# Optimization experiments

Hardware: AMD Instinct MI355X
Metric: run time of the kernel (lower is better)

## Reference

```python
import jax, jax.numpy as jnp
import numpy as np

B, T = 8, 5
C2, C1, C0 = 128, 256, 512  # in_channels = [C2, C1, C0]


def _ln(x, g, b):
    # LayerNorm over last (channel) axis
    m = jnp.mean(x, axis=-1, keepdims=True)
    v = jnp.var(x, axis=-1, keepdims=True)
    return (x - m) * jax.lax.rsqrt(v + 1e-5) * g + b


def _fuse_branch(x, gc, bc, gr, br, Wcur, Wref, bf, convw, bns, bnb):
    # x: [B, C, T, H, W]
    xt = jnp.transpose(x, (0, 2, 3, 4, 1))            # [B, T, H, W, C] (channel-last, like the permutes)
    cur = xt[:, -1]                                    # [B, H, W, C] last frame
    refs = xt[:, :-1]                                  # [B, T-1, H, W, C]
    # ShiftVSS stand-in: cross-frame fuse with residual (vectorized over T-1 frames)
    cur_proj = jnp.einsum('bhwc,cd->bhwd', _ln(cur, gc, bc), Wcur)        # [B,H,W,C]
    ref_proj = jnp.einsum('bthwc,cd->bthwd', _ln(refs, gr, br), Wref)     # [B,T-1,H,W,C]
    h = cur[:, None] + jax.nn.silu(cur_proj[:, None] + ref_proj + bf)     # [B,T-1,H,W,C]
    # BaseConv 1x1: pointwise conv + folded-BN + SiLU
    y = jax.nn.silu(jnp.einsum('bthwc,cd->bthwd', h, convw) * bns + bnb)  # [B,T-1,H,W,C]
    # fused temporal max + avg pooling (AdaptiveMax/AvgPool3d to T=1)
    pooled = jnp.max(y, axis=1) + jnp.mean(y, axis=1)                     # [B,H,W,C]
    return jnp.transpose(pooled, (0, 3, 1, 2))                            # [B,C,H,W]


def setup_inputs() -> dict:
    key = jax.random.key(0)
    ks = jax.random.split(key, 32)

    def n(k, shape, s=1.0):
        return jax.random.normal(k, shape, dtype=jnp.float32) * s

    d = {}
    d['x2'] = n(ks[0], (B, C2, T, 64, 64))
    d['x1'] = n(ks[1], (B, C1, T, 32, 32))
    d['x0'] = n(ks[2], (B, C0, T, 16, 16))  # unused by forward, kept for signature fidelity
    for i, (p, C) in enumerate([('2', C2), ('1', C1)]):
        o = 3 + i * 4
        d[f'g{p}c'] = jnp.ones((C,), jnp.float32)
        d[f'b{p}c'] = jnp.zeros((C,), jnp.float32)
        d[f'g{p}r'] = jnp.ones((C,), jnp.float32)
        d[f'b{p}r'] = jnp.zeros((C,), jnp.float32)
        d[f'W{p}cur'] = n(ks[o], (C, C), 0.02)
        d[f'W{p}ref'] = n(ks[o + 1], (C, C), 0.02)
        d[f'bias{p}'] = jnp.zeros((C,), jnp.float32)
        d[f'convw{p}'] = n(ks[o + 2], (C, C), 0.02)
        d[f'bns{p}'] = jnp.ones((C,), jnp.float32)
        d[f'bnb{p}'] = jnp.zeros((C,), jnp.float32)
    return d


def reference(x2, x1, x0,
              g2c, b2c, g2r, b2r, W2cur, W2ref, bias2, convw2, bns2, bnb2,
              g1c, b1c, g1r, b1r, W1cur, W1ref, bias1, convw1, bns1, bnb1):
    x2_out = _fuse_branch(x2, g2c, b2c, g2r, b2r, W2cur, W2ref, bias2, convw2, bns2, bnb2)
    x1_out = _fuse_branch(x1, g1c, b1c, g1r, b1r, W1cur, W1ref, bias1, convw1, bns1, bnb1)
    return (x2_out, x1_out)
```

## Files before the change

kernel.cpp:

```cpp
#include <hip/hip_runtime.h>
#include <stdint.h>

#define DI __device__ __forceinline__

typedef __attribute__((ext_vector_type(8))) short short8;
typedef __attribute__((ext_vector_type(4))) float f32x4;

DI float bf2f(unsigned short u){ union{unsigned int i; float f;} v; v.i = ((unsigned int)u)<<16; return v.f; }
DI unsigned short f2bf(float f){ union{float f; unsigned int i;} v; v.f=f; return (unsigned short)((v.i + 0x7fffu + ((v.i>>16)&1u))>>16); }
DI float siluf(float x){ return x/(1.f + __expf(-x)); }
DI f32x4 vzero(){ f32x4 z; z[0]=0.f;z[1]=0.f;z[2]=0.f;z[3]=0.f; return z; }
DI f32x4 vsplat(float x){ f32x4 z; z[0]=x;z[1]=x;z[2]=x;z[3]=x; return z; }

struct PrepArgs {
  const float* W[6];
  const float* g[6];
  unsigned short* Wt[6];
  int C[6];
};

__global__ __launch_bounds__(256) void prep_transpose(PrepArgs a){
  int m = blockIdx.z;
  int C = a.C[m];
  int nt = C >> 5;
  if ((int)blockIdx.x >= nt || (int)blockIdx.y >= nt) return;
  __shared__ float tile[32][33];
  int col = threadIdx.x & 31;
  int rr  = threadIdx.x >> 5;
  const float* W = a.W[m];
  const float* g = a.g[m];
  #pragma unroll
  for (int p=0;p<4;++p){
    int r = rr + p*8;
    int cK = blockIdx.x*32 + r;
    int dN = blockIdx.y*32 + col;
    float v = W[(size_t)cK*C + dN];
    if (g) v *= g[cK];
    tile[r][col] = v;
  }
  __syncthreads();
  unsigned short* Wt = a.Wt[m];
  #pragma unroll
  for (int p=0;p<4;++p){
    int r = rr + p*8;
    int dN = blockIdx.y*32 + r;
    int cK = blockIdx.x*32 + col;
    Wt[(size_t)dN*C + cK] = f2bf(tile[col][r]);
  }
}

struct ColArgs {
  const float* W[4]; const float* g[4]; const float* b[4]; const float* extra[4];
  float* ocs[4]; float* obs[4]; int C[4];
};

__global__ __launch_bounds__(256) void prep_colsum(ColArgs a){
  int j = blockIdx.y;
  int C = a.C[j];
  int d0 = blockIdx.x * 64;
  if (d0 >= C) return;
  int dl = threadIdx.x & 63;
  int g  = threadIdx.x >> 6;
  int d  = d0 + dl;
  const float* W = a.W[j]; const float* gv = a.g[j]; const float* bv = a.b[j];
  float cs = 0.f, bs = 0.f;
  for (int c = g; c < C; c += 4){
    float gc = gv[c], bc = bv[c];
    float w = W[(size_t)c*C + d];
    cs += gc*w;
    bs += bc*w;
  }
  __shared__ float rcs[4][64], rbs[4][64];
  rcs[g][dl] = cs; rbs[g][dl] = bs;
  __syncthreads();
  if (threadIdx.x < 64){
    float c0 = rcs[0][dl]+rcs[1][dl]+rcs[2][dl]+rcs[3][dl];
    float b0 = rbs[0][dl]+rbs[1][dl]+rbs[2][dl]+rbs[3][dl];
    if (a.extra[j]) b0 += a.extra[j][d];
    a.ocs[j][d] = c0;
    a.obs[j][d] = b0;
  }
}

template<int C, int PX>
__global__ __launch_bounds__(256) void fusedv5(
    const float* __restrict__ x,
    const unsigned short* __restrict__ WtCur,
    const unsigned short* __restrict__ WtRef,
    const unsigned short* __restrict__ WtConv,
    const float* __restrict__ colC, const float* __restrict__ biasC,
    const float* __restrict__ colR, const float* __restrict__ biasR,
    const float* __restrict__ bns, const float* __restrict__ bnb,
    float* __restrict__ out, int HW){
  constexpr int T = 5;
  constexpr int DSPAN = C/4;
  constexpr int NF = DSPAN/16;
  constexpr int MF = PX/16;
  constexpr int KS = C/32;
  constexpr int G = 256/PX;
  constexpr int PER = (C/8)/G;
  constexpr int PQn = PX/4;
  constexpr int ABYTES = PX*2*C;
  constexpr int POOLB = PX*(C+1)*4;
  constexpr int LDS_TOT = (ABYTES + 2048 + PX*8 > POOLB) ? (ABYTES + 2048 + PX*8) : POOLB;

  __shared__ __align__(16) char L[LDS_TOT];
  float* red = (float*)(L + ABYTES);
  float* smean = (float*)(L + ABYTES + 2048);
  float* srstd = smean + PX;

  int px0 = blockIdx.x*PX;
  int b = px0 / HW, hw0 = px0 % HW;
  int tid = threadIdx.x, lane = tid&63, wc = tid>>6;
  int cl = lane&15, hi = lane>>4;
  const float* xbase = x + (size_t)b*C*T*HW + hw0;

  auto loadX = [&](const float* xb, f32x4 (&p)[4]){
    #pragma unroll
    for (int i=0;i<4;++i){
      int c, pq;
      if constexpr (C==128){ c = (tid>>3) + i*32; pq = tid&7; }
      else                 { c = (tid>>2) + i*64; pq = tid&3; }
      p[i] = *(const f32x4*)(xb + (size_t)c*(T*HW) + pq*4);
    }
  };
  auto commitX = [&](const f32x4 (&p)[4]){
    #pragma unroll
    for (int i=0;i<4;++i){
      int c, pq;
      if constexpr (C==128){ c = (tid>>3) + i*32; pq = tid&7; }
      else                 { c = (tid>>2) + i*64; pq = tid&3; }
      #pragma unroll
      for (int j=0;j<4;++j){
        int px = pq*4 + j;
        *(unsigned short*)(L + px*(2*C) + (((c>>3) ^ (px&7))*16) + (c&7)*2) = f2bf(p[i][j]);
      }
    }
  };

  auto statsX = [&](){
    int px = tid & (PX-1), g = tid / PX;
    float s=0.f, q=0.f;
    #pragma unroll
    for (int k2=0;k2<PER;++k2){
      int ch = g*PER + k2;
      short8 v = *(const short8*)(L + px*(2*C) + ((ch ^ (px&7))*16));
      #pragma unroll
      for (int e=0;e<8;++e){ float f = bf2f((unsigned short)v[e]); s += f; q += f*f; }
    }
    red[g*PX+px] = s; red[256 + g*PX+px] = q;
    __syncthreads();
    if (tid < PX){
      float ss=0.f, qq=0.f;
      #pragma unroll
      for (int gg=0; gg<G; ++gg){ ss += red[gg*PX+tid]; qq += red[256+gg*PX+tid]; }
      float m = ss*(1.f/C);
      float var = fmaxf(qq*(1.f/C) - m*m, 0.f);
      smean[tid] = m;
      srstd[tid] = rsqrtf(var + 1e-5f);
    }
    __syncthreads();
  };

  auto gemm = [&](const unsigned short* __restrict__ Wt, f32x4 (&acc)[MF][NF]){
    #pragma unroll
    for (int ks=0;ks<KS;++ks){
      short8 bf8[NF];
      #pragma unroll
      for (int nf=0;nf<NF;++nf){
        int row = wc*DSPAN + nf*16 + cl;
        bf8[nf] = *(const short8*)(Wt + (size_t)row*C + ks*32 + hi*8);
      }
      short8 af[MF];
      #pragma unroll
      for (int mf=0;mf<MF;++mf){
        int row = mf*16 + cl;
        int chs = (ks*4 + hi) ^ (row&7);
        af[mf] = *(const short8*)(L + row*(2*C) + chs*16);
      }
      #pragma unroll
      for (int mf=0;mf<MF;++mf)
        #pragma unroll
        for (int nf=0;nf<NF;++nf)
          acc[mf][nf] = __builtin_amdgcn_mfma_f32_16x16x32_bf16(af[mf], bf8[nf], acc[mf][nf], 0,0,0);
    }
  };

  float csR[NF], biR[NF], scn[NF], sbn[NF];
  #pragma unroll
  for (int nf=0;nf<NF;++nf){
    int d = wc*DSPAN + nf*16 + cl;
    csR[nf] = colR[d]; biR[nf] = biasR[d];
    scn[nf] = bns[d];  sbn[nf] = bnb[d];
  }
  unsigned short pv[NF][MF*4], cvr[NF][MF*4];
  f32x4 mx[NF][MF], sm[NF][MF];
  #pragma unroll
  for (int nf=0;nf<NF;++nf)
    #pragma unroll
    for (int mf=0;mf<MF;++mf){ mx[nf][mf] = vsplat(-3.0e38f); sm[nf][mf] = vzero(); }

  f32x4 p[4];

  loadX(xbase + (size_t)(T-1)*HW, p);
  commitX(p);
  __syncthreads();
  statsX();
  loadX(xbase, p);
  {
    f32x4 acc[MF][NF];
    #pragma unroll
    for (int mf=0;mf<MF;++mf)
      #pragma unroll
      for (int nf=0;nf<NF;++nf) acc[mf][nf]=vzero();
    gemm(WtCur, acc);
    #pragma unroll
    for (int nf=0;nf<NF;++nf){
      int dg = wc*DSPAN + nf*16 + cl;
      float cs = colC[dg], bi = biasC[dg];
      #pragma unroll
      for (int mf=0;mf<MF;++mf)
        #pragma unroll
        for (int r=0;r<4;++r){
          int pl = mf*16 + hi*4 + r;
          float P = srstd[pl]*(acc[mf][nf][r] - smean[pl]*cs) + bi;
          pv[nf][mf*4+r] = f2bf(P);
          cvr[nf][mf*4+r] = *(const unsigned short*)(L + pl*(2*C) + (((dg>>3)^(pl&7))*16) + (dg&7)*2);
        }
    }
  }

  for (int t=0;t<4;++t){
    __syncthreads();
    commitX(p);
    __syncthreads();
    statsX();
    if (t < 3) loadX(xbase + (size_t)(t+1)*HW, p);

    f32x4 acc[MF][NF];
    #pragma unroll
    for (int mf=0;mf<MF;++mf)
      #pragma unroll
      for (int nf=0;nf<NF;++nf) acc[mf][nf]=vzero();
    gemm(WtRef, acc);

    __syncthreads();
    #pragma unroll
    for (int nf=0;nf<NF;++nf){
      int dg = wc*DSPAN + nf*16 + cl;
      #pragma unroll
      for (int mf=0;mf<MF;++mf)
        #pragma unroll
        for (int r=0;r<4;++r){
          int pl = mf*16 + hi*4 + r;
          float pre = srstd[pl]*(acc[mf][nf][r] - smean[pl]*csR[nf]) + biR[nf] + bf2f(pv[nf][mf*4+r]);
          float hv = bf2f(cvr[nf][mf*4+r]) + siluf(pre);
          *(unsigned short*)(L + pl*(2*C) + (((dg>>3)^(pl&7))*16) + (dg&7)*2) = f2bf(hv);
        }
    }
    __syncthreads();

    f32x4 acc2[MF][NF];
    #pragma unroll
    for (int mf=0;mf<MF;++mf)
      #pragma unroll
      for (int nf=0;nf<NF;++nf) acc2[mf][nf]=vzero();
    gemm(WtConv, acc2);
    #pragma unroll
    for (int nf=0;nf<NF;++nf)
      #pragma unroll
      for (int mf=0;mf<MF;++mf)
        #pragma unroll
        for (int r=0;r<4;++r){
          float y = siluf(acc2[mf][nf][r]*scn[nf] + sbn[nf]);
          mx[nf][mf][r] = fmaxf(mx[nf][mf][r], y);
          sm[nf][mf][r] += y;
        }
  }

  __syncthreads();
  float* pool = (float*)L;
  #pragma unroll
  for (int nf=0;nf<NF;++nf){
    int dl = wc*DSPAN + nf*16 + cl;
    #pragma unroll
    for (int mf=0;mf<MF;++mf)
      #pragma unroll
      for (int r=0;r<4;++r){
        int pl = mf*16 + hi*4 + r;
        pool[pl*(C+1) + dl] = mx[nf][mf][r] + 0.25f*sm[nf][mf][r];
      }
  }
  __syncthreads();
  #pragma unroll
  for (int it=0; it<(C*PQn)/256; ++it){
    int i = tid + it*256;
    int dl = i / PQn, pq = i % PQn;
    f32x4 vv;
    #pragma unroll
    for (int k=0;k<4;++k) vv[k] = pool[(pq*4+k)*(C+1) + dl];
    *(f32x4*)(out + (size_t)(b*C + dl)*HW + hw0 + pq*4) = vv;
  }
}

extern "C" void kernel_launch(void* const* d_in, const int* in_sizes, int n_in,
                              void* d_out, int out_size, void* d_ws, size_t ws_size,
                              hipStream_t stream) {
  (void)in_sizes; (void)n_in; (void)out_size; (void)ws_size;
  const float* x2    = (const float*)d_in[0];
  const float* x1    = (const float*)d_in[1];
  const float* g2c   = (const float*)d_in[3];
  const float* b2c   = (const float*)d_in[4];
  const float* g2r   = (const float*)d_in[5];
  const float* b2r   = (const float*)d_in[6];
  const float* W2cur = (const float*)d_in[7];
  const float* W2ref = (const float*)d_in[8];
  const float* bias2 = (const float*)d_in[9];
  const float* convw2= (const float*)d_in[10];
  const float* bns2  = (const float*)d_in[11];
  const float* bnb2  = (const float*)d_in[12];
  const float* g1c   = (const float*)d_in[13];
  const float* b1c   = (const float*)d_in[14];
  const float* g1r   = (const float*)d_in[15];
  const float* b1r   = (const float*)d_in[16];
  const float* W1cur = (const float*)d_in[17];
  const float* W1ref = (const float*)d_in[18];
  const float* bias1 = (const float*)d_in[19];
  const float* convw1= (const float*)d_in[20];
  const float* bns1  = (const float*)d_in[21];
  const float* bnb1  = (const float*)d_in[22];

  const int C2 = 128, C1 = 256;
  const int NP2 = 8*64*64, NP1 = 8*32*32;
  const int HW2 = 4096, HW1 = 1024;

  char* ws = (char*)d_ws;
  size_t off = 0;
  auto alloc = [&](size_t bytes){ size_t o = off; off = (off + bytes + 255) & ~(size_t)255; return o; };
  size_t oWtC2 = alloc((size_t)C2*C2*2), oWtR2 = alloc((size_t)C2*C2*2), oWtV2 = alloc((size_t)C2*C2*2);
  size_t oWtC1 = alloc((size_t)C1*C1*2), oWtR1 = alloc((size_t)C1*C1*2), oWtV1 = alloc((size_t)C1*C1*2);
  size_t oColC2 = alloc(C2*4), oBiasC2 = alloc(C2*4), oColR2 = alloc(C2*4), oBiasR2 = alloc(C2*4);
  size_t oColC1 = alloc(C1*4), oBiasC1 = alloc(C1*4), oColR1 = alloc(C1*4), oBiasR1 = alloc(C1*4);

  unsigned short* WtC2 = (unsigned short*)(ws + oWtC2);
  unsigned short* WtR2 = (unsigned short*)(ws + oWtR2);
  unsigned short* WtV2 = (unsigned short*)(ws + oWtV2);
  unsigned short* WtC1 = (unsigned short*)(ws + oWtC1);
  unsigned short* WtR1 = (unsigned short*)(ws + oWtR1);
  unsigned short* WtV1 = (unsigned short*)(ws + oWtV1);
  float* ColC2 = (float*)(ws + oColC2); float* BiasC2 = (float*)(ws + oBiasC2);
  float* ColR2 = (float*)(ws + oColR2); float* BiasR2 = (float*)(ws + oBiasR2);
  float* ColC1 = (float*)(ws + oColC1); float* BiasC1 = (float*)(ws + oBiasC1);
  float* ColR1 = (float*)(ws + oColR1); float* BiasR1 = (float*)(ws + oBiasR1);

  PrepArgs pa;
  pa.W[0]=W2cur;  pa.g[0]=g2c;     pa.Wt[0]=WtC2; pa.C[0]=C2;
  pa.W[1]=W2ref;  pa.g[1]=g2r;     pa.Wt[1]=WtR2; pa.C[1]=C2;
  pa.W[2]=convw2; pa.g[2]=nullptr; pa.Wt[2]=WtV2; pa.C[2]=C2;
  pa.W[3]=W1cur;  pa.g[3]=g1c;     pa.Wt[3]=WtC1; pa.C[3]=C1;
  pa.W[4]=W1ref;  pa.g[4]=g1r;     pa.Wt[4]=WtR1; pa.C[4]=C1;
  pa.W[5]=convw1; pa.g[5]=nullptr; pa.Wt[5]=WtV1; pa.C[5]=C1;
  prep_transpose<<<dim3(8,8,6), 256, 0, stream>>>(pa);

  ColArgs ca;
  ca.W[0]=W2cur; ca.g[0]=g2c; ca.b[0]=b2c; ca.extra[0]=nullptr; ca.ocs[0]=ColC2; ca.obs[0]=BiasC2; ca.C[0]=C2;
  ca.W[1]=W2ref; ca.g[1]=g2r; ca.b[1]=b2r; ca.extra[1]=bias2;   ca.ocs[1]=ColR2; ca.obs[1]=BiasR2; ca.C[1]=C2;
  ca.W[2]=W1cur; ca.g[2]=g1c; ca.b[2]=b1c; ca.extra[2]=nullptr; ca.ocs[2]=ColC1; ca.obs[2]=BiasC1; ca.C[2]=C1;
  ca.W[3]=W1ref; ca.g[3]=g1r; ca.b[3]=b1r; ca.extra[3]=bias1;   ca.ocs[3]=ColR1; ca.obs[3]=BiasR1; ca.C[3]=C1;
  prep_colsum<<<dim3(4, 4), 256, 0, stream>>>(ca);

  float* out2 = (float*)d_out;
  float* out1 = out2 + (size_t)8*C2*HW2;

  fusedv5<128,32><<<NP2/32, 256, 0, stream>>>(
      x2, WtC2, WtR2, WtV2, ColC2, BiasC2, ColR2, BiasR2, bns2, bnb2, out2, HW2);
  fusedv5<256,16><<<NP1/16, 256, 0, stream>>>(
      x1, WtC1, WtR1, WtV1, ColC1, BiasC1, ColR1, BiasR1, bns1, bnb1, out1, HW1);
}
```

Baseline: 146.9 us.

## Merge both branch kernels into one launch and compute LN stats from registers

```diff
diff --git a/kernel.cpp b/kernel.cpp
--- a/kernel.cpp
+++ b/kernel.cpp
@@ -82,78 +82,91 @@
   }
 }
 
+struct BranchArgs {
+  const float* x;
+  const unsigned short* WtCur;
+  const unsigned short* WtRef;
+  const unsigned short* WtConv;
+  const float* colC; const float* biasC;
+  const float* colR; const float* biasR;
+  const float* bns;  const float* bnb;
+  float* out; int HW;
+};
+
+constexpr int LDS_BYTES = 19072;
+
 template<int C, int PX>
-__global__ __launch_bounds__(256) void fusedv5(
-    const float* __restrict__ x,
-    const unsigned short* __restrict__ WtCur,
-    const unsigned short* __restrict__ WtRef,
-    const unsigned short* __restrict__ WtConv,
-    const float* __restrict__ colC, const float* __restrict__ biasC,
-    const float* __restrict__ colR, const float* __restrict__ biasR,
-    const float* __restrict__ bns, const float* __restrict__ bnb,
-    float* __restrict__ out, int HW){
+DI void fused_body(const BranchArgs& a, int bx, char* L){
   constexpr int T = 5;
   constexpr int DSPAN = C/4;
   constexpr int NF = DSPAN/16;
   constexpr int MF = PX/16;
   constexpr int KS = C/32;
+  constexpr int PQN = PX/4;
+  constexpr int C0N = 256/PQN;
   constexpr int G = 256/PX;
-  constexpr int PER = (C/8)/G;
-  constexpr int PQn = PX/4;
-  constexpr int ABYTES = PX*2*C;
-  constexpr int POOLB = PX*(C+1)*4;
-  constexpr int LDS_TOT = (ABYTES + 2048 + PX*8 > POOLB) ? (ABYTES + 2048 + PX*8) : POOLB;
-
-  __shared__ __align__(16) char L[LDS_TOT];
-  float* red = (float*)(L + ABYTES);
-  float* smean = (float*)(L + ABYTES + 2048);
+  constexpr int CPG = C0N/G;
+
+  short* As = (short*)L;
+  float* redS = (float*)(L + PX*2*C);
+  float* redQ = redS + C0N*(PX+1);
+  float* red2S = redQ + C0N*(PX+1);
+  float* red2Q = red2S + 256;
+  float* smean = red2Q + 256;
   float* srstd = smean + PX;
 
-  int px0 = blockIdx.x*PX;
+  int HW = a.HW;
+  int px0 = bx*PX;
   int b = px0 / HW, hw0 = px0 % HW;
   int tid = threadIdx.x, lane = tid&63, wc = tid>>6;
   int cl = lane&15, hi = lane>>4;
-  const float* xbase = x + (size_t)b*C*T*HW + hw0;
+  int pq = tid & (PQN-1);
+  int c0 = tid / PQN;
+  const float* xbase = a.x + (size_t)b*C*T*HW + hw0;
 
   auto loadX = [&](const float* xb, f32x4 (&p)[4]){
     #pragma unroll
     for (int i=0;i<4;++i){
-      int c, pq;
-      if constexpr (C==128){ c = (tid>>3) + i*32; pq = tid&7; }
-      else                 { c = (tid>>2) + i*64; pq = tid&3; }
+      int c = c0*4 + i;
       p[i] = *(const f32x4*)(xb + (size_t)c*(T*HW) + pq*4);
     }
   };
   auto commitX = [&](const f32x4 (&p)[4]){
     #pragma unroll
     for (int i=0;i<4;++i){
-      int c, pq;
-      if constexpr (C==128){ c = (tid>>3) + i*32; pq = tid&7; }
-      else                 { c = (tid>>2) + i*64; pq = tid&3; }
+      int c = c0*4 + i;
       #pragma unroll
       for (int j=0;j<4;++j){
         int px = pq*4 + j;
         *(unsigned short*)(L + px*(2*C) + (((c>>3) ^ (px&7))*16) + (c&7)*2) = f2bf(p[i][j]);
       }
     }
+    #pragma unroll
+    for (int j=0;j<4;++j){
+      float s = p[0][j]+p[1][j]+p[2][j]+p[3][j];
+      float q = p[0][j]*p[0][j]+p[1][j]*p[1][j]+p[2][j]*p[2][j]+p[3][j]*p[3][j];
+      int px = pq*4 + j;
+      redS[c0*(PX+1) + px] = s;
+      redQ[c0*(PX+1) + px] = q;
+    }
   };
-
-  auto statsX = [&](){
-    int px = tid & (PX-1), g = tid / PX;
-    float s=0.f, q=0.f;
-    #pragma unroll
-    for (int k2=0;k2<PER;++k2){
-      int ch = g*PER + k2;
-      short8 v = *(const short8*)(L + px*(2*C) + ((ch ^ (px&7))*16));
-      #pragma unroll
-      for (int e=0;e<8;++e){ float f = bf2f((unsigned short)v[e]); s += f; q += f*f; }
-    }
-    red[g*PX+px] = s; red[256 + g*PX+px] = q;
+  auto reduceStats = [&](){
+    {
+      int px = tid & (PX-1), g = tid / PX;
+      float s=0.f, q=0.f;
+      #pragma unroll
+      for (int k=0;k<CPG;++k){
+        int cc = g*CPG + k;
+        s += redS[cc*(PX+1) + px];
+        q += redQ[cc*(PX+1) + px];
+      }
+      red2S[g*PX+px] = s; red2Q[g*PX+px] = q;
+    }
     __syncthreads();
     if (tid < PX){
       float ss=0.f, qq=0.f;
       #pragma unroll
-      for (int gg=0; gg<G; ++gg){ ss += red[gg*PX+tid]; qq += red[256+gg*PX+tid]; }
+      for (int g=0;g<G;++g){ ss += red2S[g*PX+tid]; qq += red2Q[g*PX+tid]; }
       float m = ss*(1.f/C);
       float var = fmaxf(qq*(1.f/C) - m*m, 0.f);
       smean[tid] = m;
@@ -190,8 +203,8 @@
   #pragma unroll
   for (int nf=0;nf<NF;++nf){
     int d = wc*DSPAN + nf*16 + cl;
-    csR[nf] = colR[d]; biR[nf] = biasR[d];
-    scn[nf] = bns[d];  sbn[nf] = bnb[d];
+    csR[nf] = a.colR[d]; biR[nf] = a.biasR[d];
+    scn[nf] = a.bns[d];  sbn[nf] = a.bnb[d];
   }
   unsigned short pv[NF][MF*4], cvr[NF][MF*4];
   f32x4 mx[NF][MF], sm[NF][MF];
@@ -205,7 +218,7 @@
   loadX(xbase + (size_t)(T-1)*HW, p);
   commitX(p);
   __syncthreads();
-  statsX();
+  reduceStats();
   loadX(xbase, p);
   {
     f32x4 acc[MF][NF];
@@ -213,11 +226,11 @@
     for (int mf=0;mf<MF;++mf)
       #pragma unroll
       for (int nf=0;nf<NF;++nf) acc[mf][nf]=vzero();
-    gemm(WtCur, acc);
+    gemm(a.WtCur, acc);
     #pragma unroll
     for (int nf=0;nf<NF;++nf){
       int dg = wc*DSPAN + nf*16 + cl;
-      float cs = colC[dg], bi = biasC[dg];
+      float cs = a.colC[dg], bi = a.biasC[dg];
       #pragma unroll
       for (int mf=0;mf<MF;++mf)
         #pragma unroll
@@ -234,7 +247,7 @@
     __syncthreads();
     commitX(p);
     __syncthreads();
-    statsX();
+    reduceStats();
     if (t < 3) loadX(xbase + (size_t)(t+1)*HW, p);
 
     f32x4 acc[MF][NF];
@@ -242,7 +255,7 @@
     for (int mf=0;mf<MF;++mf)
       #pragma unroll
       for (int nf=0;nf<NF;++nf) acc[mf][nf]=vzero();
-    gemm(WtRef, acc);
+    gemm(a.WtRef, acc);
 
     __syncthreads();
     #pragma unroll
@@ -265,7 +278,7 @@
     for (int mf=0;mf<MF;++mf)
       #pragma unroll
       for (int nf=0;nf<NF;++nf) acc2[mf][nf]=vzero();
-    gemm(WtConv, acc2);
+    gemm(a.WtConv, acc2);
     #pragma unroll
     for (int nf=0;nf<NF;++nf)
       #pragma unroll
@@ -293,14 +306,21 @@
   }
   __syncthreads();
   #pragma unroll
-  for (int it=0; it<(C*PQn)/256; ++it){
+  for (int it=0; it<(C*PQN)/256; ++it){
     int i = tid + it*256;
-    int dl = i / PQn, pq = i % PQn;
+    int dl = i / PQN, pq2 = i % PQN;
     f32x4 vv;
     #pragma unroll
-    for (int k=0;k<4;++k) vv[k] = pool[(pq*4+k)*(C+1) + dl];
-    *(f32x4*)(out + (size_t)(b*C + dl)*HW + hw0 + pq*4) = vv;
-  }
+    for (int k=0;k<4;++k) vv[k] = pool[(pq2*4+k)*(C+1) + dl];
+    *(f32x4*)(a.out + (size_t)(b*C + dl)*HW + hw0 + pq2*4) = vv;
+  }
+}
+
+__global__ __launch_bounds__(256) void fused_all(BranchArgs a1 , BranchArgs a2 , int NB1){
+  __shared__ __align__(16) char L[LDS_BYTES];
+  int bx = blockIdx.x;
+  if (bx < NB1) fused_body<256,16>(a1, bx, L);
+  else          fused_body<128,32>(a2, bx - NB1, L);
 }
 
 extern "C" void kernel_launch(void* const* d_in, const int* in_sizes, int n_in,
@@ -372,8 +392,10 @@
   float* out2 = (float*)d_out;
   float* out1 = out2 + (size_t)8*C2*HW2;
 
-  fusedv5<128,32><<<NP2/32, 256, 0, stream>>>(
-      x2, WtC2, WtR2, WtV2, ColC2, BiasC2, ColR2, BiasR2, bns2, bnb2, out2, HW2);
-  fusedv5<256,16><<<NP1/16, 256, 0, stream>>>(
-      x1, WtC1, WtR1, WtV1, ColC1, BiasC1, ColR1, BiasR1, bns1, bnb1, out1, HW1);
+  BranchArgs a2b{ x2, WtC2, WtR2, WtV2, ColC2, BiasC2, ColR2, BiasR2, bns2, bnb2, out2, HW2 };
+  BranchArgs a1b{ x1, WtC1, WtR1, WtV1, ColC1, BiasC1, ColR1, BiasR1, bns1, bnb1, out1, HW1 };
+
+  const int NB1 = NP1/16;
+  const int NB2 = NP2/32;
+  fused_all<<<NB1 + NB2, 256, 0, stream>>>(a1b, a2b, NB1);
 }
```

Result: slower. 202.5 us (+37.8%).
